# Kernel tuning notes

Hardware: AMD Instinct MI355X
Metric: run time of the kernel (lower is better)

Reference implementation:

```python
import math
import jax, jax.numpy as jnp
import numpy as np

D_IN = 768      # input_hidden_dim
H = 512         # IDLU_hidden_dim
E = 64          # num_entity
B = 32          # batch_size (mentions)
P = 197         # num_patch (incl. CLS)
RHO = 4.0
EPS = 1e-5


def setup_inputs() -> dict:
    key = jax.random.key(0)
    ks = jax.random.split(key, 16)
    s = 1.0 / math.sqrt(D_IN)
    return {
        "entity_cls": jax.random.normal(ks[0], (E, D_IN), jnp.float32),
        "entity_tokens": jax.random.normal(ks[1], (E, P, D_IN), jnp.float32),
        "mention_image_cls": jax.random.normal(ks[2], (B, D_IN), jnp.float32),
        "mention_image_tokens": jax.random.normal(ks[3], (B, P, D_IN), jnp.float32),
        "mention_patch_mask": jax.random.uniform(ks[4], (B, P), jnp.float32),
        "Wq": jax.random.normal(ks[5], (D_IN, H), jnp.float32) * s,
        "bq": jnp.zeros((H,), jnp.float32),
        "Wk": jax.random.normal(ks[6], (D_IN, H), jnp.float32) * s,
        "bk": jnp.zeros((H,), jnp.float32),
        "Wv": jax.random.normal(ks[7], (D_IN, H), jnp.float32) * s,
        "bv": jnp.zeros((H,), jnp.float32),
        "Wcls": jax.random.normal(ks[8], (D_IN, H), jnp.float32) * s,
        "bcls": jnp.zeros((H,), jnp.float32),
        "ln_g": jnp.ones((H,), jnp.float32),
        "ln_b": jnp.zeros((H,), jnp.float32),
    }


def _layer_norm(x, g, b):
    mu = jnp.mean(x, axis=-1, keepdims=True)
    var = jnp.mean(jnp.square(x - mu), axis=-1, keepdims=True)
    return (x - mu) * jax.lax.rsqrt(var + EPS) * g + b


def reference(entity_cls, entity_tokens, mention_image_cls, mention_image_tokens,
              mention_patch_mask, Wq, bq, Wk, bk, Wv, bv, Wcls, bcls, ln_g, ln_b):
    entity_cls_fc = entity_cls @ Wcls + bcls                      # [E, H]
    q = entity_tokens @ Wq + bq                                   # [E, P, H]
    k = mention_image_tokens @ Wk + bk                            # [B, P, H]
    v = mention_image_tokens @ Wv + bv                            # [B, P, H]
    # broadcast entity x mention attention: [E, B, P, P]
    scores = jnp.einsum('eph,bqh->ebpq', q, k) / math.sqrt(H)
    # additive mask only on the first query row (CLS)
    scores = scores.at[:, :, 0, :].add(RHO * mention_patch_mask[None, :, :])
    probs = jax.nn.softmax(scores, axis=-1)                       # [E, B, P, P]
    context = jnp.einsum('ebpq,bqh->ebph', probs, v)              # [E, B, P, H]
    context = jnp.mean(context, axis=-2)                          # [E, B, H]
    context = _layer_norm(context, ln_g, ln_b)
    g2l = jnp.sum(entity_cls_fc[:, None, :] * context, axis=-1).T # [B, E]
    g2g = mention_image_cls @ entity_cls.T                        # [B, E]
    return (g2l + g2g) / 2
```

## Files before the change

kernel.cpp:

```cpp
#include <hip/hip_runtime.h>
#include <stdint.h>

#define EN 64
#define BN 32
#define PN 197
#define DIN 768
#define HH 512
#define RHO_ 4.0f

typedef __attribute__((ext_vector_type(8))) short bf16x8;
typedef __attribute__((ext_vector_type(4))) float f32x4;

__device__ __forceinline__ ushort f2bf(float f){
  unsigned u = __float_as_uint(f);
  u += 0x7FFFu + ((u >> 16) & 1u);
  return (ushort)(u >> 16);
}
__device__ __forceinline__ float bf2f(ushort h){ return __uint_as_float(((unsigned)h) << 16); }

__global__ __launch_bounds__(256) void prep_kernel(
    const float* __restrict__ etok, const float* __restrict__ mtok,
    const float* __restrict__ ecls, const float* __restrict__ bq,
    ushort* __restrict__ a_ent, ushort* __restrict__ a_men, ushort* __restrict__ a_cls,
    float* __restrict__ bq_s)
{
  int g = blockIdx.x*256 + threadIdx.x;
  int st = gridDim.x*256;
  const float s = 0.04419417382415922f;
  for (int i=g; i<(EN*PN*DIN)/4; i+=st){
    float4 v = ((const float4*)etok)[i];
    ushort4 o; o.x=f2bf(v.x); o.y=f2bf(v.y); o.z=f2bf(v.z); o.w=f2bf(v.w);
    ((ushort4*)a_ent)[i] = o;
  }
  for (int i=g; i<(BN*PN*DIN)/4; i+=st){
    float4 v = ((const float4*)mtok)[i];
    ushort4 o; o.x=f2bf(v.x); o.y=f2bf(v.y); o.z=f2bf(v.z); o.w=f2bf(v.w);
    ((ushort4*)a_men)[i] = o;
  }
  for (int i=g; i<(EN*DIN)/4; i+=st){
    float4 v = ((const float4*)ecls)[i];
    ushort4 o; o.x=f2bf(v.x); o.y=f2bf(v.y); o.z=f2bf(v.z); o.w=f2bf(v.w);
    ((ushort4*)a_cls)[i] = o;
  }
  for (int i=g; i<HH; i+=st) bq_s[i] = bq[i]*s;
}

__global__ __launch_bounds__(256) void w_transpose(
    const float* __restrict__ Wq, const float* __restrict__ Wk,
    const float* __restrict__ Wv, const float* __restrict__ Wc,
    ushort* __restrict__ Wt)
{
  __shared__ float tl[64][65];
  int mat = blockIdx.z;
  const float* src = (mat==0)?Wq:(mat==1)?Wk:(mat==2)?Wv:Wc;
  float sc = (mat==0)? 0.04419417382415922f : 1.0f;
  int k0 = blockIdx.x*64;
  int n0 = blockIdx.y*64;
  int tid = threadIdx.x;
  int c = tid & 63, r0 = tid >> 6;
  #pragma unroll
  for (int i=0;i<16;++i){
    int r = r0 + i*4;
    tl[r][c] = src[(size_t)(k0+r)*HH + n0+c];
  }
  __syncthreads();
  ushort* dst = Wt + (size_t)mat*HH*DIN;
  #pragma unroll
  for (int i=0;i<16;++i){
    int r = r0 + i*4;
    dst[(size_t)(n0+r)*DIN + k0+c] = f2bf(tl[c][r]*sc);
  }
}

__global__ __launch_bounds__(256) void gemm_proj(
    const ushort* __restrict__ a_ent, const ushort* __restrict__ a_men, const ushort* __restrict__ a_cls,
    const ushort* __restrict__ Wt,
    const float* __restrict__ bq_s, const float* __restrict__ bk,
    const float* __restrict__ bv, const float* __restrict__ bc,
    ushort* __restrict__ qo, ushort* __restrict__ ko, ushort* __restrict__ vo,
    float* __restrict__ co)
{
  int x = blockIdx.x;
  int op, mt;
  if (x < 99)        { op = 0; mt = x; }
  else if (x < 149)  { op = 1; mt = x - 99; }
  else if (x < 199)  { op = 2; mt = x - 149; }
  else               { op = 3; mt = 0; }
  int M = (op==0)? EN*PN : (op==3)? EN : BN*PN;
  int m0 = mt*128;
  const ushort* A  = (op==0)? a_ent : (op==3)? a_cls : a_men;
  const ushort* Bw = Wt + (size_t)op*HH*DIN;
  const float* bias = (op==0)? bq_s : (op==1)? bk : (op==2)? bv : bc;
  int n0 = blockIdx.y*128;
  int Mm1 = M-1;

  __shared__ ushort As[128*40];
  __shared__ ushort Bs[128*40];
  int tid = threadIdx.x;
  int lane = tid & 63, wid = tid >> 6;
  int l15 = lane & 15, lg = lane >> 4;
  int wm = wid >> 1, wn = wid & 1;

  f32x4 acc[16];
  #pragma unroll
  for (int i=0;i<16;++i){ f32x4 z = {0.f,0.f,0.f,0.f}; acc[i] = z; }

  bf16x8 sA[2], sB[2];
  #pragma unroll
  for (int i=0;i<2;++i){
    int u = tid + i*256; int row = u>>2; int ko8 = (u&3)*8;
    int rA = m0+row; rA = rA>Mm1 ? Mm1 : rA;
    sA[i] = *(const bf16x8*)(A  + (size_t)rA*DIN + ko8);
    sB[i] = *(const bf16x8*)(Bw + (size_t)(n0+row)*DIN + ko8);
  }
  for (int kt=0; kt<DIN/32; ++kt){
    #pragma unroll
    for (int i=0;i<2;++i){
      int u = tid + i*256; int row = u>>2; int ko8 = (u&3)*8;
      *(bf16x8*)(&As[row*40 + ko8]) = sA[i];
      *(bf16x8*)(&Bs[row*40 + ko8]) = sB[i];
    }
    __syncthreads();
    if (kt < DIN/32 - 1){
      int k0 = (kt+1)*32;
      #pragma unroll
      for (int i=0;i<2;++i){
        int u = tid + i*256; int row = u>>2; int ko8 = (u&3)*8;
        int rA = m0+row; rA = rA>Mm1 ? Mm1 : rA;
        sA[i] = *(const bf16x8*)(A  + (size_t)rA*DIN + k0 + ko8);
        sB[i] = *(const bf16x8*)(Bw + (size_t)(n0+row)*DIN + k0 + ko8);
      }
    }
    bf16x8 af[4], bfg[4];
    #pragma unroll
    for (int t=0;t<4;++t){
      af[t]  = *(const bf16x8*)(&As[(wm*64 + t*16 + l15)*40 + lg*8]);
      bfg[t] = *(const bf16x8*)(&Bs[(wn*64 + t*16 + l15)*40 + lg*8]);
    }
    #pragma unroll
    for (int am=0; am<4; ++am)
      #pragma unroll
      for (int bn=0; bn<4; ++bn)
        acc[am*4+bn] = __builtin_amdgcn_mfma_f32_16x16x32_bf16(af[am], bfg[bn], acc[am*4+bn], 0, 0, 0);
    __syncthreads();
  }

  #pragma unroll
  for (int bn=0; bn<4; ++bn){
    int col = n0 + wn*64 + bn*16 + l15;
    float bval = bias[col];
    #pragma unroll
    for (int am=0; am<4; ++am){
      #pragma unroll
      for (int r=0;r<4;++r){
        int row = m0 + wm*64 + am*16 + lg*4 + r;
        if (row < M){
          float v = acc[am*4+bn][r] + bval;
          if (op==3)      co[(size_t)row*HH + col] = v;
          else if (op==0) qo[(size_t)row*HH + col] = f2bf(v);
          else if (op==1) ko[(size_t)row*HH + col] = f2bf(v);
          else            vo[(size_t)row*HH + col] = f2bf(v);
        }
      }
    }
  }
}

__global__ __launch_bounds__(512) void attn_kernel(
    const ushort* __restrict__ qw, const ushort* __restrict__ kw, const ushort* __restrict__ vw,
    const float* __restrict__ cls_fc, const float* __restrict__ maskp,
    const float* __restrict__ mcls, const float* __restrict__ ecls,
    const float* __restrict__ lng, const float* __restrict__ lnb,
    float* __restrict__ outp)
{
  int bid = blockIdx.x;
  int b = bid >> 5;
  int e0 = (bid & 31) * 2;

  __shared__ ushort klds[2][112*256];
  __shared__ float w_lds[2][208];
  __shared__ float red[32];

  int tid = threadIdx.x;
  int lane = tid & 63, wid = tid >> 6;
  int l15 = lane & 15, lg = (lane >> 4) & 3;

  for (int i=tid; i<416; i+=512) ((float*)w_lds)[i] = 0.f;

  const ushort* kb  = kw + (size_t)b*PN*HH;
  const ushort* qb0 = qw + (size_t)e0*PN*HH;
  const ushort* qb1 = qw + (size_t)(e0+1)*PN*HH;

  bf16x8 stg[7];
  bf16x8 afr[2][8];

  for (int rnd=0; rnd<2; ++rnd){
    int tt = rnd*8 + wid;
    bool active = tt < 13;
    int rt = active ? tt : 12;
    int arow = rt*16 + l15;
    int arowg = arow > 196 ? 196 : arow;

    f32x4 acc[2][13];
    #pragma unroll
    for (int e2=0;e2<2;++e2)
      #pragma unroll
      for (int i=0;i<13;++i){ f32x4 z={0.f,0.f,0.f,0.f}; acc[e2][i]=z; }

    #pragma unroll
    for (int i=0;i<7;++i){
      int u = tid + i*512; int col = u>>5, o32 = u&31;
      int cg = col > 196 ? 196 : col;
      stg[i] = *(const bf16x8*)(kb + (size_t)cg*HH + o32*8);
    }

    for (int c=0; c<4; ++c){
      int kh = c>>1, ch = c&1;
      __syncthreads();
      #pragma unroll
      for (int i=0;i<7;++i){
        int u = tid + i*512; int col = u>>5, o32 = u&31;
        *(bf16x8*)(&klds[ch][col*256 + ((o32 ^ (col&7))*8)]) = stg[i];
      }
      __syncthreads();
      if (c < 3){
        int nkh = (c+1)>>1, ncb = ((c+1)&1)*112;
        #pragma unroll
        for (int i=0;i<7;++i){
          int u = tid + i*512; int col = u>>5, o32 = u&31;
          int cg = ncb + col; cg = cg > 196 ? 196 : cg;
          stg[i] = *(const bf16x8*)(kb + (size_t)cg*HH + nkh*256 + o32*8);
        }
      }
      if (ch == 0 && active){
        #pragma unroll
        for (int lc=0; lc<8; ++lc){
          afr[0][lc] = *(const bf16x8*)(qb0 + (size_t)arowg*HH + kh*256 + lc*32 + lg*8);
          afr[1][lc] = *(const bf16x8*)(qb1 + (size_t)arowg*HH + kh*256 + lc*32 + lg*8);
        }
      }
      if (active){
        if (ch == 0){
          #pragma unroll
          for (int ct=0; ct<7; ++ct){
            int lcol = ct*16 + l15, sw = lcol & 7;
            #pragma unroll
            for (int lc=0; lc<8; ++lc){
              bf16x8 bfr = *(const bf16x8*)(&klds[0][lcol*256 + (((lc*4+lg) ^ sw)*8)]);
              acc[0][ct] = __builtin_amdgcn_mfma_f32_16x16x32_bf16(afr[0][lc], bfr, acc[0][ct], 0,0,0);
              acc[1][ct] = __builtin_amdgcn_mfma_f32_16x16x32_bf16(afr[1][lc], bfr, acc[1][ct], 0,0,0);
            }
          }
        } else {
          #pragma unroll
          for (int ct=0; ct<6; ++ct){
            int lcol = ct*16 + l15, sw = lcol & 7;
            #pragma unroll
            for (int lc=0; lc<8; ++lc){
              bf16x8 bfr = *(const bf16x8*)(&klds[1][lcol*256 + (((lc*4+lg) ^ sw)*8)]);
              acc[0][7+ct] = __builtin_amdgcn_mfma_f32_16x16x32_bf16(afr[0][lc], bfr, acc[0][7+ct], 0,0,0);
              acc[1][7+ct] = __builtin_amdgcn_mfma_f32_16x16x32_bf16(afr[1][lc], bfr, acc[1][7+ct], 0,0,0);
            }
          }
        }
      }
    }

    if (active){
      #pragma unroll
      for (int e2=0; e2<2; ++e2){
        if (l15 >= 5){
          f32x4 ninf = {-1e30f,-1e30f,-1e30f,-1e30f};
          acc[e2][12] = ninf;
        }
        if (rt==0 && lg==0){
          #pragma unroll
          for (int ct=0; ct<13; ++ct){
            int col = ct*16 + l15;
            if (col < 197) acc[e2][ct][0] += RHO_ * maskp[b*PN + col];
          }
        }
        float mrow[4], inv[4];
        #pragma unroll
        for (int r=0;r<4;++r){
          float m = acc[e2][0][r];
          #pragma unroll
          for (int ct=1; ct<13; ++ct) m = fmaxf(m, acc[e2][ct][r]);
          m = fmaxf(m, __shfl_xor(m,1));
          m = fmaxf(m, __shfl_xor(m,2));
          m = fmaxf(m, __shfl_xor(m,4));
          m = fmaxf(m, __shfl_xor(m,8));
          mrow[r] = m;
        }
        #pragma unroll
        for (int r=0;r<4;++r){
          float s = 0.f;
          #pragma unroll
          for (int ct=0; ct<13; ++ct){
            float ev = __expf(acc[e2][ct][r] - mrow[r]);
            acc[e2][ct][r] = ev;
            s += ev;
          }
          s += __shfl_xor(s,1); s += __shfl_xor(s,2);
          s += __shfl_xor(s,4); s += __shfl_xor(s,8);
          int prow = rt*16 + lg*4 + r;
          inv[r] = (prow < PN) ? 1.0f/s : 0.f;
        }
        #pragma unroll
        for (int ct=0; ct<13; ++ct){
          float cs = acc[e2][ct][0]*inv[0] + acc[e2][ct][1]*inv[1]
                   + acc[e2][ct][2]*inv[2] + acc[e2][ct][3]*inv[3];
          cs += __shfl_xor(cs,16);
          cs += __shfl_xor(cs,32);
          if (lg==0) atomicAdd(&w_lds[e2][ct*16 + l15], cs);
        }
      }
    }
  }
  __syncthreads();

  const ushort* vb = vw + (size_t)b*PN*HH;
  float cA=0.f, cB=0.f;
  #pragma unroll 4
  for (int q=0; q<PN; ++q){
    float vq = bf2f(vb[(size_t)q*HH + tid]);
    cA += w_lds[0][q]*vq;
    cB += w_lds[1][q]*vq;
  }
  const float invP = 1.0f/197.0f;
  cA*=invP; cB*=invP;

  float sx = cA, sxx = cA*cA, sy = cB, syy = cB*cB;
  #pragma unroll
  for (int off=32; off; off>>=1){
    sx += __shfl_down(sx, off); sxx += __shfl_down(sxx, off);
    sy += __shfl_down(sy, off); syy += __shfl_down(syy, off);
  }
  if (lane==0){ red[wid*4+0]=sx; red[wid*4+1]=sxx; red[wid*4+2]=sy; red[wid*4+3]=syy; }
  __syncthreads();
  float s1A=0.f, s2A=0.f, s1B=0.f, s2B=0.f;
  #pragma unroll
  for (int w=0; w<8; ++w){
    s1A += red[w*4+0]; s2A += red[w*4+1];
    s1B += red[w*4+2]; s2B += red[w*4+3];
  }
  float muA = s1A*(1.f/512.f), muB = s1B*(1.f/512.f);
  float varA = s2A*(1.f/512.f) - muA*muA;
  float varB = s2B*(1.f/512.f) - muB*muB;
  float rsA = rsqrtf(varA + 1e-5f), rsB = rsqrtf(varB + 1e-5f);

  int h = tid;
  float g0=lng[h], bb0=lnb[h];
  float dA = ((cA-muA)*rsA*g0 + bb0) * cls_fc[(size_t)e0*HH + h];
  float dB = ((cB-muB)*rsB*g0 + bb0) * cls_fc[(size_t)(e0+1)*HH + h];

  dA += mcls[b*DIN + tid]*ecls[(size_t)e0*DIN + tid];
  dB += mcls[b*DIN + tid]*ecls[(size_t)(e0+1)*DIN + tid];
  if (tid < 256){
    int j = tid + 512;
    dA += mcls[b*DIN + j]*ecls[(size_t)e0*DIN + j];
    dB += mcls[b*DIN + j]*ecls[(size_t)(e0+1)*DIN + j];
  }

  __syncthreads();
  #pragma unroll
  for (int off=32; off; off>>=1){ dA += __shfl_down(dA, off); dB += __shfl_down(dB, off); }
  if (lane==0){ red[wid*2+0]=dA; red[wid*2+1]=dB; }
  __syncthreads();
  if (tid==0){
    float oA=0.f, oB=0.f;
    #pragma unroll
    for (int w=0; w<8; ++w){ oA += red[w*2+0]; oB += red[w*2+1]; }
    outp[b*EN + e0]   = 0.5f*oA;
    outp[b*EN + e0+1] = 0.5f*oB;
  }
}

extern "C" void kernel_launch(void* const* d_in, const int* in_sizes, int n_in,
                              void* d_out, int out_size, void* d_ws, size_t ws_size,
                              hipStream_t stream)
{
  (void)in_sizes; (void)n_in; (void)out_size; (void)ws_size;
  const float* ecls = (const float*)d_in[0];
  const float* etok = (const float*)d_in[1];
  const float* mcls = (const float*)d_in[2];
  const float* mtok = (const float*)d_in[3];
  const float* maskp= (const float*)d_in[4];
  const float* Wq   = (const float*)d_in[5];
  const float* bq   = (const float*)d_in[6];
  const float* Wk   = (const float*)d_in[7];
  const float* bk   = (const float*)d_in[8];
  const float* Wv   = (const float*)d_in[9];
  const float* bv   = (const float*)d_in[10];
  const float* Wc   = (const float*)d_in[11];
  const float* bc   = (const float*)d_in[12];
  const float* lng  = (const float*)d_in[13];
  const float* lnb  = (const float*)d_in[14];

  char* ws = (char*)d_ws;
  size_t off = 0;
  auto take = [&](size_t bytes){ char* p = ws + off; off += (bytes + 255) & ~(size_t)255; return p; };
  ushort* a_ent = (ushort*)take((size_t)EN*PN*DIN*2);
  ushort* a_men = (ushort*)take((size_t)BN*PN*DIN*2);
  ushort* a_cls = (ushort*)take((size_t)EN*DIN*2);
  ushort* Wt    = (ushort*)take((size_t)4*HH*DIN*2);
  float*  bq_s  = (float*)take((size_t)HH*4);
  ushort* qo    = (ushort*)take((size_t)EN*PN*HH*2);
  ushort* ko    = (ushort*)take((size_t)BN*PN*HH*2);
  ushort* vo    = (ushort*)take((size_t)BN*PN*HH*2);
  float*  co    = (float*)take((size_t)EN*HH*4);

  prep_kernel<<<1024, 256, 0, stream>>>(etok, mtok, ecls, bq, a_ent, a_men, a_cls, bq_s);
  w_transpose<<<dim3(12,8,4), 256, 0, stream>>>(Wq, Wk, Wv, Wc, Wt);
  gemm_proj<<<dim3(200,4,1), 256, 0, stream>>>(a_ent, a_men, a_cls, Wt,
                                               bq_s, bk, bv, bc, qo, ko, vo, co);
  attn_kernel<<<1024, 512, 0, stream>>>(qo, ko, vo, co, maskp, mcls, ecls,
                                        lng, lnb, (float*)d_out);
}
```

Baseline: 554.9 us.

## Stream K tiles into LDS via direct global-to-LDS loads with prefetch

Replaces the register-staged K tile copy with global_load_lds direct DMA into a double-buffered LDS tile. The swizzle is applied on the source address instead of the LDS address. The loop order is swapped so Q fragments are loaded per-k-step with one-ahead prefetch instead of holding 16 fragments in registers, which lowers VGPR pressure and drops one barrier per chunk. The risk is that only a single __syncthreads may not wait for outstanding LDS DMA (vmcnt) before reading the buffer, and the rolled lc loop adds latency from global Q loads.

Result: faster. 481.9 us (-13.2%).

```diff
diff --git a/kernel.cpp b/kernel.cpp
--- a/kernel.cpp
+++ b/kernel.cpp
@@ -17,6 +17,10 @@
   return (ushort)(u >> 16);
 }
 __device__ __forceinline__ float bf2f(ushort h){ return __uint_as_float(((unsigned)h) << 16); }
+
+#define GLOAD_LDS16(g, l) __builtin_amdgcn_global_load_lds( \
+    (const __attribute__((address_space(1))) void*)(g), \
+    (__attribute__((address_space(3))) void*)(l), 16, 0, 0)
 
 __global__ __launch_bounds__(256) void prep_kernel(
     const float* __restrict__ etok, const float* __restrict__ mtok,
@@ -191,8 +195,17 @@
   const ushort* qb0 = qw + (size_t)e0*PN*HH;
   const ushort* qb1 = qw + (size_t)(e0+1)*PN*HH;
 
-  bf16x8 stg[7];
-  bf16x8 afr[2][8];
+  auto issue = [&](int ch, int kh, int cb){
+    #pragma unroll
+    for (int i=0;i<7;++i){
+      int L   = tid + i*512;
+      int col = L >> 5, j = L & 31;
+      int cg  = cb + col; cg = cg > 196 ? 196 : cg;
+      const ushort* src = kb + (size_t)cg*HH + kh*256 + ((j ^ (col & 7)) * 8);
+      ushort* dst = &klds[ch][ (size_t)(wid*64 + i*512) * 8 ];
+      GLOAD_LDS16(src, dst);
+    }
+  };
 
   for (int rnd=0; rnd<2; ++rnd){
     int tt = rnd*8 + wid;
@@ -207,59 +220,51 @@
       #pragma unroll
       for (int i=0;i<13;++i){ f32x4 z={0.f,0.f,0.f,0.f}; acc[e2][i]=z; }
 
-    #pragma unroll
-    for (int i=0;i<7;++i){
-      int u = tid + i*512; int col = u>>5, o32 = u&31;
-      int cg = col > 196 ? 196 : col;
-      stg[i] = *(const bf16x8*)(kb + (size_t)cg*HH + o32*8);
-    }
+    const ushort* q0base = qb0 + (size_t)arowg*HH + lg*8;
+    const ushort* q1base = qb1 + (size_t)arowg*HH + lg*8;
+
+    if (rnd==0) issue(0, 0, 0);
 
     for (int c=0; c<4; ++c){
       int kh = c>>1, ch = c&1;
       __syncthreads();
-      #pragma unroll
-      for (int i=0;i<7;++i){
-        int u = tid + i*512; int col = u>>5, o32 = u&31;
-        *(bf16x8*)(&klds[ch][col*256 + ((o32 ^ (col&7))*8)]) = stg[i];
-      }
-      __syncthreads();
-      if (c < 3){
-        int nkh = (c+1)>>1, ncb = ((c+1)&1)*112;
-        #pragma unroll
-        for (int i=0;i<7;++i){
-          int u = tid + i*512; int col = u>>5, o32 = u&31;
-          int cg = ncb + col; cg = cg > 196 ? 196 : cg;
-          stg[i] = *(const bf16x8*)(kb + (size_t)cg*HH + nkh*256 + o32*8);
-        }
-      }
-      if (ch == 0 && active){
-        #pragma unroll
-        for (int lc=0; lc<8; ++lc){
-          afr[0][lc] = *(const bf16x8*)(qb0 + (size_t)arowg*HH + kh*256 + lc*32 + lg*8);
-          afr[1][lc] = *(const bf16x8*)(qb1 + (size_t)arowg*HH + kh*256 + lc*32 + lg*8);
-        }
-      }
+      if (c < 3)            issue(ch^1, (c+1)>>1, ((c+1)&1)*112);
+      else if (rnd == 0)    issue(0, 0, 0);
       if (active){
+        const ushort* q0 = q0base + kh*256;
+        const ushort* q1 = q1base + kh*256;
+        bf16x8 a0 = *(const bf16x8*)q0;
+        bf16x8 a1 = *(const bf16x8*)q1;
         if (ch == 0){
-          #pragma unroll
-          for (int ct=0; ct<7; ++ct){
-            int lcol = ct*16 + l15, sw = lcol & 7;
+          #pragma unroll 1
+          for (int lc=0; lc<8; ++lc){
+            bf16x8 c0 = a0, c1 = a1;
+            int nx = (lc<7 ? lc+1 : lc)*32;
+            a0 = *(const bf16x8*)(q0 + nx);
+            a1 = *(const bf16x8*)(q1 + nx);
+            int ru = lc*4 + lg;
             #pragma unroll
-            for (int lc=0; lc<8; ++lc){
-              bf16x8 bfr = *(const bf16x8*)(&klds[0][lcol*256 + (((lc*4+lg) ^ sw)*8)]);
-              acc[0][ct] = __builtin_amdgcn_mfma_f32_16x16x32_bf16(afr[0][lc], bfr, acc[0][ct], 0,0,0);
-              acc[1][ct] = __builtin_amdgcn_mfma_f32_16x16x32_bf16(afr[1][lc], bfr, acc[1][ct], 0,0,0);
+            for (int ct=0; ct<7; ++ct){
+              int lcol = ct*16 + l15;
+              bf16x8 bfr = *(const bf16x8*)(&klds[0][lcol*256 + ((ru ^ (lcol&7))*8)]);
+              acc[0][ct] = __builtin_amdgcn_mfma_f32_16x16x32_bf16(c0, bfr, acc[0][ct], 0,0,0);
+              acc[1][ct] = __builtin_amdgcn_mfma_f32_16x16x32_bf16(c1, bfr, acc[1][ct], 0,0,0);
             }
           }
         } else {
-          #pragma unroll
-          for (int ct=0; ct<6; ++ct){
-            int lcol = ct*16 + l15, sw = lcol & 7;
+          #pragma unroll 1
+          for (int lc=0; lc<8; ++lc){
+            bf16x8 c0 = a0, c1 = a1;
+            int nx = (lc<7 ? lc+1 : lc)*32;
+            a0 = *(const bf16x8*)(q0 + nx);
+            a1 = *(const bf16x8*)(q1 + nx);
+            int ru = lc*4 + lg;
             #pragma unroll
-            for (int lc=0; lc<8; ++lc){
-              bf16x8 bfr = *(const bf16x8*)(&klds[1][lcol*256 + (((lc*4+lg) ^ sw)*8)]);
-              acc[0][7+ct] = __builtin_amdgcn_mfma_f32_16x16x32_bf16(afr[0][lc], bfr, acc[0][7+ct], 0,0,0);
-              acc[1][7+ct] = __builtin_amdgcn_mfma_f32_16x16x32_bf16(afr[1][lc], bfr, acc[1][7+ct], 0,0,0);
+            for (int ct=0; ct<6; ++ct){
+              int lcol = ct*16 + l15;
+              bf16x8 bfr = *(const bf16x8*)(&klds[1][lcol*256 + ((ru ^ (lcol&7))*8)]);
+              acc[0][7+ct] = __builtin_amdgcn_mfma_f32_16x16x32_bf16(c0, bfr, acc[0][7+ct], 0,0,0);
+              acc[1][7+ct] = __builtin_amdgcn_mfma_f32_16x16x32_bf16(c1, bfr, acc[1][7+ct], 0,0,0);
             }
           }
         }
```

## Stream K tiles via direct global-to-LDS loads with finer double-buffered K chunks

Applied to the files above, without the earlier changes.

Replaces the register-staged K tile loading (global to registers, then to LDS, with two barriers per chunk) with global_load_lds direct-to-LDS transfers, using 64-wide K chunks across all 197 columns in a double buffer with one barrier per step. Q fragments are now prefetched one chunk ahead in registers instead of loading 8 fragments per half, which cuts register pressure. The two row-tile rounds are flattened into a single 16-step pipelined loop. This aims to overlap K loading with MFMA work and reduce LDS staging overhead, at the cost of more barriers overall and reliance on the async LDS load path's ordering.

New measurement: 472.9 us. -14.8%, faster.

```diff
diff --git a/kernel.cpp b/kernel.cpp
--- a/kernel.cpp
+++ b/kernel.cpp
@@ -17,6 +17,10 @@
   return (ushort)(u >> 16);
 }
 __device__ __forceinline__ float bf2f(ushort h){ return __uint_as_float(((unsigned)h) << 16); }
+
+#define GLOAD_LDS16(g, l) __builtin_amdgcn_global_load_lds( \
+    (const __attribute__((address_space(1))) void*)(g), \
+    (__attribute__((address_space(3))) void*)(l), 16, 0, 0)
 
 __global__ __launch_bounds__(256) void prep_kernel(
     const float* __restrict__ etok, const float* __restrict__ mtok,
@@ -177,7 +181,7 @@
   int b = bid >> 5;
   int e0 = (bid & 31) * 2;
 
-  __shared__ ushort klds[2][112*256];
+  __shared__ ushort klds[2][1664*8];
   __shared__ float w_lds[2][208];
   __shared__ float red[32];
 
@@ -187,133 +191,138 @@
 
   for (int i=tid; i<416; i+=512) ((float*)w_lds)[i] = 0.f;
 
-  const ushort* kb  = kw + (size_t)b*PN*HH;
+  const ushort* kb = kw + (size_t)b*PN*HH;
   const ushort* qb0 = qw + (size_t)e0*PN*HH;
   const ushort* qb1 = qw + (size_t)(e0+1)*PN*HH;
 
-  bf16x8 stg[7];
-  bf16x8 afr[2][8];
-
-  for (int rnd=0; rnd<2; ++rnd){
+  auto issue = [&](int bf, int kc){
+    #pragma unroll
+    for (int i=0;i<4;++i){
+      int L = tid + i*512;
+      if (L < 1664){
+        int col = L >> 3, j = L & 7;
+        int cg = col > 196 ? 196 : col;
+        const ushort* src = kb + (size_t)cg*HH + kc*64 + ((j ^ (col & 7)) * 8);
+        ushort* dst = &klds[bf][ (wid*64 + i*512) * 8 ];
+        GLOAD_LDS16(src, dst);
+      }
+    }
+  };
+
+  int ar0 = wid*16 + l15;
+  int tt1 = 8 + wid;
+  int rt1 = tt1 > 12 ? 12 : tt1;
+  int ar1 = rt1*16 + l15; ar1 = ar1 > 196 ? 196 : ar1;
+  const ushort* q00 = qb0 + (size_t)ar0*HH + lg*8;
+  const ushort* q01 = qb1 + (size_t)ar0*HH + lg*8;
+  const ushort* q10 = qb0 + (size_t)ar1*HH + lg*8;
+  const ushort* q11 = qb1 + (size_t)ar1*HH + lg*8;
+
+  f32x4 acc[2][13];
+  #pragma unroll
+  for (int e2=0;e2<2;++e2)
+    #pragma unroll
+    for (int i=0;i<13;++i){ f32x4 z={0.f,0.f,0.f,0.f}; acc[e2][i]=z; }
+
+  issue(0, 0);
+  bf16x8 qc[2][2], qn[2][2];
+  #pragma unroll
+  for (int s=0; s<2; ++s){
+    qc[0][s] = *(const bf16x8*)(q00 + s*32);
+    qc[1][s] = *(const bf16x8*)(q01 + s*32);
+  }
+
+  #pragma unroll 1
+  for (int g=0; g<16; ++g){
+    int rnd = g >> 3, c = g & 7;
+    __syncthreads();
+    if (g < 15){
+      issue((g+1)&1, (g+1)&7);
+      int nkc = (g+1)&7;
+      const ushort* a0 = ((g+1)>>3) ? q10 : q00;
+      const ushort* a1 = ((g+1)>>3) ? q11 : q01;
+      #pragma unroll
+      for (int s=0; s<2; ++s){
+        qn[0][s] = *(const bf16x8*)(a0 + nkc*64 + s*32);
+        qn[1][s] = *(const bf16x8*)(a1 + nkc*64 + s*32);
+      }
+    }
     int tt = rnd*8 + wid;
     bool active = tt < 13;
-    int rt = active ? tt : 12;
-    int arow = rt*16 + l15;
-    int arowg = arow > 196 ? 196 : arow;
-
-    f32x4 acc[2][13];
-    #pragma unroll
-    for (int e2=0;e2<2;++e2)
+    if (active){
+      const ushort* kbase = &klds[g&1][0];
       #pragma unroll
-      for (int i=0;i<13;++i){ f32x4 z={0.f,0.f,0.f,0.f}; acc[e2][i]=z; }
-
-    #pragma unroll
-    for (int i=0;i<7;++i){
-      int u = tid + i*512; int col = u>>5, o32 = u&31;
-      int cg = col > 196 ? 196 : col;
-      stg[i] = *(const bf16x8*)(kb + (size_t)cg*HH + o32*8);
-    }
-
-    for (int c=0; c<4; ++c){
-      int kh = c>>1, ch = c&1;
-      __syncthreads();
-      #pragma unroll
-      for (int i=0;i<7;++i){
-        int u = tid + i*512; int col = u>>5, o32 = u&31;
-        *(bf16x8*)(&klds[ch][col*256 + ((o32 ^ (col&7))*8)]) = stg[i];
-      }
-      __syncthreads();
-      if (c < 3){
-        int nkh = (c+1)>>1, ncb = ((c+1)&1)*112;
+      for (int s=0; s<2; ++s){
+        int ru = s*4 + lg;
         #pragma unroll
-        for (int i=0;i<7;++i){
-          int u = tid + i*512; int col = u>>5, o32 = u&31;
-          int cg = ncb + col; cg = cg > 196 ? 196 : cg;
-          stg[i] = *(const bf16x8*)(kb + (size_t)cg*HH + nkh*256 + o32*8);
+        for (int ct=0; ct<13; ++ct){
+          int lcol = ct*16 + l15;
+          bf16x8 bfr = *(const bf16x8*)(kbase + (size_t)(lcol*8 + (ru ^ (lcol&7)))*8);
+          acc[0][ct] = __builtin_amdgcn_mfma_f32_16x16x32_bf16(qc[0][s], bfr, acc[0][ct], 0,0,0);
+          acc[1][ct] = __builtin_amdgcn_mfma_f32_16x16x32_bf16(qc[1][s], bfr, acc[1][ct], 0,0,0);
         }
       }
-      if (ch == 0 && active){
+    }
+    #pragma unroll
+    for (int s=0; s<2; ++s){ qc[0][s] = qn[0][s]; qc[1][s] = qn[1][s]; }
+
+    if (c == 7){
+      if (active){
+        int rt = tt > 12 ? 12 : tt;
         #pragma unroll
-        for (int lc=0; lc<8; ++lc){
-          afr[0][lc] = *(const bf16x8*)(qb0 + (size_t)arowg*HH + kh*256 + lc*32 + lg*8);
-          afr[1][lc] = *(const bf16x8*)(qb1 + (size_t)arowg*HH + kh*256 + lc*32 + lg*8);
-        }
-      }
-      if (active){
-        if (ch == 0){
-          #pragma unroll
-          for (int ct=0; ct<7; ++ct){
-            int lcol = ct*16 + l15, sw = lcol & 7;
+        for (int e2=0; e2<2; ++e2){
+          if (l15 >= 5){
+            f32x4 ninf = {-1e30f,-1e30f,-1e30f,-1e30f};
+            acc[e2][12] = ninf;
+          }
+          if (rt==0 && lg==0){
             #pragma unroll
-            for (int lc=0; lc<8; ++lc){
-              bf16x8 bfr = *(const bf16x8*)(&klds[0][lcol*256 + (((lc*4+lg) ^ sw)*8)]);
-              acc[0][ct] = __builtin_amdgcn_mfma_f32_16x16x32_bf16(afr[0][lc], bfr, acc[0][ct], 0,0,0);
-              acc[1][ct] = __builtin_amdgcn_mfma_f32_16x16x32_bf16(afr[1][lc], bfr, acc[1][ct], 0,0,0);
+            for (int ct=0; ct<13; ++ct){
+              int col = ct*16 + l15;
+              if (col < 197) acc[e2][ct][0] += RHO_ * maskp[b*PN + col];
             }
           }
-        } else {
+          float mrow[4], inv[4];
           #pragma unroll
-          for (int ct=0; ct<6; ++ct){
-            int lcol = ct*16 + l15, sw = lcol & 7;
+          for (int r=0;r<4;++r){
+            float m = acc[e2][0][r];
             #pragma unroll
-            for (int lc=0; lc<8; ++lc){
-              bf16x8 bfr = *(const bf16x8*)(&klds[1][lcol*256 + (((lc*4+lg) ^ sw)*8)]);
-              acc[0][7+ct] = __builtin_amdgcn_mfma_f32_16x16x32_bf16(afr[0][lc], bfr, acc[0][7+ct], 0,0,0);
-              acc[1][7+ct] = __builtin_amdgcn_mfma_f32_16x16x32_bf16(afr[1][lc], bfr, acc[1][7+ct], 0,0,0);
+            for (int ct=1; ct<13; ++ct) m = fmaxf(m, acc[e2][ct][r]);
+            m = fmaxf(m, __shfl_xor(m,1));
+            m = fmaxf(m, __shfl_xor(m,2));
+            m = fmaxf(m, __shfl_xor(m,4));
+            m = fmaxf(m, __shfl_xor(m,8));
+            mrow[r] = m;
+          }
+          #pragma unroll
+          for (int r=0;r<4;++r){
+            float sm = 0.f;
+            #pragma unroll
+            for (int ct=0; ct<13; ++ct){
+              float ev = __expf(acc[e2][ct][r] - mrow[r]);
+              acc[e2][ct][r] = ev;
+              sm += ev;
             }
+            sm += __shfl_xor(sm,1); sm += __shfl_xor(sm,2);
+            sm += __shfl_xor(sm,4); sm += __shfl_xor(sm,8);
+            int prow = rt*16 + lg*4 + r;
+            inv[r] = (prow < PN) ? 1.0f/sm : 0.f;
+          }
+          #pragma unroll
+          for (int ct=0; ct<13; ++ct){
+            float cs = acc[e2][ct][0]*inv[0] + acc[e2][ct][1]*inv[1]
+                     + acc[e2][ct][2]*inv[2] + acc[e2][ct][3]*inv[3];
+            cs += __shfl_xor(cs,16);
+            cs += __shfl_xor(cs,32);
+            if (lg==0) atomicAdd(&w_lds[e2][ct*16 + l15], cs);
           }
         }
       }
-    }
-
-    if (active){
-      #pragma unroll
-      for (int e2=0; e2<2; ++e2){
-        if (l15 >= 5){
-          f32x4 ninf = {-1e30f,-1e30f,-1e30f,-1e30f};
-          acc[e2][12] = ninf;
-        }
-        if (rt==0 && lg==0){
+      if (rnd == 0){
+        #pragma unroll
+        for (int e2=0;e2<2;++e2)
           #pragma unroll
-          for (int ct=0; ct<13; ++ct){
-            int col = ct*16 + l15;
-            if (col < 197) acc[e2][ct][0] += RHO_ * maskp[b*PN + col];
-          }
-        }
-        float mrow[4], inv[4];
-        #pragma unroll
-        for (int r=0;r<4;++r){
-          float m = acc[e2][0][r];
-          #pragma unroll
-          for (int ct=1; ct<13; ++ct) m = fmaxf(m, acc[e2][ct][r]);
-          m = fmaxf(m, __shfl_xor(m,1));
-          m = fmaxf(m, __shfl_xor(m,2));
-          m = fmaxf(m, __shfl_xor(m,4));
-          m = fmaxf(m, __shfl_xor(m,8));
-          mrow[r] = m;
-        }
-        #pragma unroll
-        for (int r=0;r<4;++r){
-          float s = 0.f;
-          #pragma unroll
-          for (int ct=0; ct<13; ++ct){
-            float ev = __expf(acc[e2][ct][r] - mrow[r]);
-            acc[e2][ct][r] = ev;
-            s += ev;
-          }
-          s += __shfl_xor(s,1); s += __shfl_xor(s,2);
-          s += __shfl_xor(s,4); s += __shfl_xor(s,8);
-          int prow = rt*16 + lg*4 + r;
-          inv[r] = (prow < PN) ? 1.0f/s : 0.f;
-        }
-        #pragma unroll
-        for (int ct=0; ct<13; ++ct){
-          float cs = acc[e2][ct][0]*inv[0] + acc[e2][ct][1]*inv[1]
-                   + acc[e2][ct][2]*inv[2] + acc[e2][ct][3]*inv[3];
-          cs += __shfl_xor(cs,16);
-          cs += __shfl_xor(cs,32);
-          if (lg==0) atomicAdd(&w_lds[e2][ct*16 + l15], cs);
-        }
+          for (int i=0;i<13;++i){ f32x4 z={0.f,0.f,0.f,0.f}; acc[e2][i]=z; }
       }
     }
   }
```
